# Kernel optimization log

Measured on AMD Instinct MI355X. Metric: run time of the kernel, lower is better.

The kernel has to match this reference:

```python
import jax, jax.numpy as jnp
import numpy as np

E = 1024
H = 16
D = E // H  # projection_dim = 64


def setup_inputs() -> dict:
    key = jax.random.key(0)
    ks = jax.random.split(key, 9)
    s = 1.0 / np.sqrt(E)
    return {
        "inputs": jax.random.normal(ks[0], (2, 2048, E), dtype=jnp.float32),
        "Wq": jax.random.uniform(ks[1], (E, E), jnp.float32, -s, s),
        "bq": jax.random.uniform(ks[2], (E,), jnp.float32, -s, s),
        "Wk": jax.random.uniform(ks[3], (E, E), jnp.float32, -s, s),
        "bk": jax.random.uniform(ks[4], (E,), jnp.float32, -s, s),
        "Wv": jax.random.uniform(ks[5], (E, E), jnp.float32, -s, s),
        "bv": jax.random.uniform(ks[6], (E,), jnp.float32, -s, s),
        "Wo": jax.random.uniform(ks[7], (E, E), jnp.float32, -s, s),
        "bo": jax.random.uniform(ks[8], (E,), jnp.float32, -s, s),
    }


def reference(inputs, Wq, bq, Wk, bk, Wv, bv, Wo, bo):
    B, S, _ = inputs.shape
    # Linear layers use y = x @ W.T + b (torch convention); weights here stored as [E,E]
    q = inputs @ Wq.T + bq
    k = inputs @ Wk.T + bk
    v = inputs @ Wv.T + bv
    # separate heads: [B,S,E] -> [B,H,S,D]
    q = q.reshape(B, S, H, D).transpose(0, 2, 1, 3)
    k = k.reshape(B, S, H, D).transpose(0, 2, 1, 3)
    v = v.reshape(B, S, H, D).transpose(0, 2, 1, 3)
    scale = 1.0 / jnp.sqrt(jnp.float32(D))
    scores = jnp.einsum('bhqd,bhkd->bhqk', q, k) * scale  # [B,H,S,S]
    weights = jax.nn.softmax(scores, axis=-1)
    attn = jnp.einsum('bhqk,bhkd->bhqd', weights, v)  # [B,H,S,D]
    concat = attn.transpose(0, 2, 1, 3).reshape(B, S, E)
    # dropout is identity in eval mode
    return concat @ Wo.T + bo
```

## Files before the change

kernel.cpp:

```cpp
#include <hip/hip_runtime.h>
#include <hip/hip_bf16.h>
#include <stdint.h>

#define E_ 1024
#define H_ 16
#define D_ 64
#define B_ 2
#define S_ 2048
#define M_ 4096

typedef __bf16 bf16_t;
typedef __bf16 bf16x8 __attribute__((ext_vector_type(8)));
typedef __bf16 bf16x4 __attribute__((ext_vector_type(4)));
typedef __bf16 bf16x2 __attribute__((ext_vector_type(2)));
typedef float  f32x4  __attribute__((ext_vector_type(4)));
typedef float  f32x16 __attribute__((ext_vector_type(16)));
typedef unsigned int u32x2 __attribute__((ext_vector_type(2)));
typedef unsigned int u32x4 __attribute__((ext_vector_type(4)));

__global__ __launch_bounds__(256) void cvt_all(
    const float* __restrict__ x,
    const float* __restrict__ w0, const float* __restrict__ w1,
    const float* __restrict__ w2, const float* __restrict__ w3,
    bf16_t* __restrict__ xd,
    bf16_t* __restrict__ d0, bf16_t* __restrict__ d1,
    bf16_t* __restrict__ d2, bf16_t* __restrict__ d3) {
  int i = blockIdx.x * blockDim.x + threadIdx.x;
  const float* src;
  bf16_t* dst;
  int off;
  if (i < (1 << 20)) {
    src = x; dst = xd; off = i;
  } else {
    int j = i - (1 << 20);
    int z = j >> 18;
    off = j & ((1 << 18) - 1);
    src = (z == 0) ? w0 : (z == 1) ? w1 : (z == 2) ? w2 : w3;
    dst = (z == 0) ? d0 : (z == 1) ? d1 : (z == 2) ? d2 : d3;
  }
  float4 v = reinterpret_cast<const float4*>(src)[off];
  bf16x4 o;
  o[0] = (bf16_t)v.x; o[1] = (bf16_t)v.y; o[2] = (bf16_t)v.z; o[3] = (bf16_t)v.w;
  reinterpret_cast<bf16x4*>(dst)[off] = o;
}

static __device__ __forceinline__ void gl_lds16(const bf16_t* g, bf16_t* l) {
  __builtin_amdgcn_global_load_lds((__attribute__((address_space(1))) void*)g,
                                   (__attribute__((address_space(3))) void*)l,
                                   16, 0, 0);
}

template <int SWAP>
static __device__ __forceinline__ void gemm128_mainloop(
    const bf16_t* __restrict__ Ag, const bf16_t* __restrict__ Bg,
    bf16_t* ldsA0, bf16_t* ldsA1, bf16_t* ldsB0, bf16_t* ldsB1,
    int m0, int n0, f32x4 acc[4][4]) {
  const int tid  = threadIdx.x;
  const int lane = tid & 63, wave = tid >> 6;
  const int lrow = lane & 15, lgrp = lane >> 4;
  const int wr = (wave >> 1) * 64, wc = (wave & 1) * 64;
  const int skol = (lane & 3) * 8;
  const int c0 = wave * 2;
  const int rowA = c0 * 16 + (lane >> 2);
  const f32x4 zero = {0.f, 0.f, 0.f, 0.f};
#pragma unroll
  for (int i = 0; i < 4; i++)
#pragma unroll
    for (int j = 0; j < 4; j++) acc[i][j] = zero;

  gl_lds16(Ag + (size_t)(m0 + rowA) * E_ + skol,      ldsA0 + c0 * 512);
  gl_lds16(Ag + (size_t)(m0 + rowA + 16) * E_ + skol, ldsA0 + (c0 + 1) * 512);
  gl_lds16(Bg + (size_t)(n0 + rowA) * E_ + skol,      ldsB0 + c0 * 512);
  gl_lds16(Bg + (size_t)(n0 + rowA + 16) * E_ + skol, ldsB0 + (c0 + 1) * 512);
  __syncthreads();

  for (int kt = 0; kt < E_ / 32; ++kt) {
    bf16_t* sA = (kt & 1) ? ldsA1 : ldsA0;
    bf16_t* sB = (kt & 1) ? ldsB1 : ldsB0;
    if (kt + 1 < E_ / 32) {
      bf16_t* dA = (kt & 1) ? ldsA0 : ldsA1;
      bf16_t* dB = (kt & 1) ? ldsB0 : ldsB1;
      const int k0 = (kt + 1) * 32;
      gl_lds16(Ag + (size_t)(m0 + rowA) * E_ + k0 + skol,      dA + c0 * 512);
      gl_lds16(Ag + (size_t)(m0 + rowA + 16) * E_ + k0 + skol, dA + (c0 + 1) * 512);
      gl_lds16(Bg + (size_t)(n0 + rowA) * E_ + k0 + skol,      dB + c0 * 512);
      gl_lds16(Bg + (size_t)(n0 + rowA + 16) * E_ + k0 + skol, dB + (c0 + 1) * 512);
    }
    bf16x8 fA[4], fB[4];
#pragma unroll
    for (int i = 0; i < 4; i++)
      fA[i] = *reinterpret_cast<const bf16x8*>(sA + (wr + i * 16 + lrow) * 32 + lgrp * 8);
#pragma unroll
    for (int j = 0; j < 4; j++)
      fB[j] = *reinterpret_cast<const bf16x8*>(sB + (wc + j * 16 + lrow) * 32 + lgrp * 8);
#pragma unroll
    for (int i = 0; i < 4; i++)
#pragma unroll
      for (int j = 0; j < 4; j++)
        acc[i][j] = SWAP
          ? __builtin_amdgcn_mfma_f32_16x16x32_bf16(fB[j], fA[i], acc[i][j], 0, 0, 0)
          : __builtin_amdgcn_mfma_f32_16x16x32_bf16(fA[i], fB[j], acc[i][j], 0, 0, 0);
    __syncthreads();
  }
}

__global__ __launch_bounds__(256) void qkv_gemm(
    const bf16_t* __restrict__ xbf, const bf16_t* __restrict__ Wqkv,
    const float* __restrict__ bq, const float* __restrict__ bk, const float* __restrict__ bv,
    bf16_t* __restrict__ Qo, bf16_t* __restrict__ Kf, bf16_t* __restrict__ Vf) {
  __shared__ alignas(16) bf16_t ldsA[2][128 * 32];
  __shared__ alignas(16) bf16_t ldsB[2][128 * 32];
  const int m0 = blockIdx.x * 128, n0 = blockIdx.y * 128;
  const int z = n0 >> 10;
  const float* bias = (z == 0) ? bq : ((z == 1) ? bk : bv);
  const int lane = threadIdx.x & 63, wave = threadIdx.x >> 6;
  const int lrow = lane & 15, lgrp = lane >> 4;
  const int wr = (wave >> 1) * 64, wc = (wave & 1) * 64;
  f32x4 acc[4][4];

  if (z == 2) {
    gemm128_mainloop<0>(xbf, Wqkv, ldsA[0], ldsA[1], ldsB[0], ldsB[1], m0, n0, acc);
#pragma unroll
    for (int i = 0; i < 4; i++) {
      const int mbase = m0 + wr + i * 16 + lgrp * 4;
      const int b = mbase >> 11, kv = mbase & (S_ - 1);
      const int t = kv >> 6, st = (kv >> 4) & 3, hi2 = (kv >> 3) & 1, j0 = kv & 7;
#pragma unroll
      for (int j = 0; j < 4; j++) {
        const int n = (n0 & 1023) + wc + j * 16 + lrow;
        const float bn = bias[n];
        const int h = n >> 6, d = n & 63;
        const int hh = d >> 5, lane2 = (hi2 << 5) | (d & 31);
        bf16x4 v;
#pragma unroll
        for (int r = 0; r < 4; r++) v[r] = (bf16_t)(acc[i][j][r] + bn);
        const size_t off = ((((size_t)(b * H_ + h) * 32 + t) * 8 + hh * 4 + st) * 64 + lane2) * 8 + j0;
        *reinterpret_cast<bf16x4*>(Vf + off) = v;
      }
    }
  } else if (z == 1) {
    gemm128_mainloop<1>(xbf, Wqkv, ldsA[0], ldsA[1], ldsB[0], ldsB[1], m0, n0, acc);
#pragma unroll
    for (int i = 0; i < 4; i++) {
      const int m = m0 + wr + i * 16 + lrow;
      const int b = m >> 11, kv = m & (S_ - 1);
      const int t = kv >> 6, hh = (kv >> 5) & 1, qll = kv & 31;
#pragma unroll
      for (int j = 0; j < 4; j++) {
        const int nb = (n0 & 1023) + wc + j * 16 + lgrp * 4;
        const int h = nb >> 6, d = nb & 63;
        const int ds = d >> 4, hi2 = (d >> 3) & 1, el = d & 7;
        const int lane2 = (hi2 << 5) | qll;
        const f32x4 b4 = *reinterpret_cast<const f32x4*>(bias + nb);
        bf16x4 v;
#pragma unroll
        for (int r = 0; r < 4; r++) v[r] = (bf16_t)(acc[i][j][r] + b4[r]);
        const size_t off = ((((size_t)(b * H_ + h) * 32 + t) * 8 + hh * 4 + ds) * 64 + lane2) * 8 + el;
        *reinterpret_cast<bf16x4*>(Kf + off) = v;
      }
    }
  } else {
    gemm128_mainloop<1>(xbf, Wqkv, ldsA[0], ldsA[1], ldsB[0], ldsB[1], m0, n0, acc);
    const float scale = 0.18033688011112042f;
#pragma unroll
    for (int i = 0; i < 4; i++) {
      const int m = m0 + wr + i * 16 + lrow;
      const int b = m >> 11, s = m & (S_ - 1);
#pragma unroll
      for (int j = 0; j < 4; j++) {
        const int nb = (n0 & 1023) + wc + j * 16 + lgrp * 4;
        const int h = nb >> 6, d = nb & 63;
        const f32x4 b4 = *reinterpret_cast<const f32x4*>(bias + nb);
        bf16x4 v;
#pragma unroll
        for (int r = 0; r < 4; r++) v[r] = (bf16_t)((acc[i][j][r] + b4[r]) * scale);
        *reinterpret_cast<bf16x4*>(Qo + ((size_t)((b * H_ + h) * S_) + s) * D_ + d) = v;
      }
    }
  }
}

__global__ __launch_bounds__(256) void out_gemm(
    const bf16_t* __restrict__ Cbf, const bf16_t* __restrict__ Wob,
    const float* __restrict__ bo, float* __restrict__ out) {
  __shared__ alignas(16) bf16_t ldsA[2][128 * 32];
  __shared__ alignas(16) bf16_t ldsB[2][128 * 32];
  const int m0 = blockIdx.x * 128, n0 = blockIdx.y * 128;
  f32x4 acc[4][4];
  gemm128_mainloop<1>(Cbf, Wob, ldsA[0], ldsA[1], ldsB[0], ldsB[1], m0, n0, acc);

  const int lane = threadIdx.x & 63, wave = threadIdx.x >> 6;
  const int lrow = lane & 15, lgrp = lane >> 4;
  const int wr = (wave >> 1) * 64, wc = (wave & 1) * 64;
#pragma unroll
  for (int i = 0; i < 4; i++) {
    const int m = m0 + wr + i * 16 + lrow;
#pragma unroll
    for (int j = 0; j < 4; j++) {
      const int nb = n0 + wc + j * 16 + lgrp * 4;
      const f32x4 b4 = *reinterpret_cast<const f32x4*>(bo + nb);
      f32x4 v = acc[i][j] + b4;
      *reinterpret_cast<f32x4*>(out + (size_t)m * E_ + nb) = v;
    }
  }
}


static __device__ __forceinline__ unsigned pack2(float a, float b) {
  bf16x2 t; t[0] = (bf16_t)a; t[1] = (bf16_t)b;
  return __builtin_bit_cast(unsigned, t);
}

static __device__ __forceinline__ bf16x8 mkfrag(unsigned a0, unsigned a1,
                                                unsigned a2, unsigned a3) {
  u32x2 s02 = __builtin_amdgcn_permlane32_swap(a0, a2, false, false);
  u32x2 s13 = __builtin_amdgcn_permlane32_swap(a1, a3, false, false);
  u32x4 t; t[0] = s02[0]; t[1] = s13[0]; t[2] = s02[1]; t[3] = s13[1];
  return *reinterpret_cast<bf16x8*>(&t);
}

__global__ __launch_bounds__(512) void attn_kernel(
    const bf16_t* __restrict__ Qg, const bf16_t* __restrict__ Kfg,
    const bf16_t* __restrict__ Vfg, bf16_t* __restrict__ Og) {
  __shared__ alignas(16) f32x4 smO[8 * 256];
  __shared__ float smL[256];
  const int f = blockIdx.x;
  const int bh = (f & 7) * 4 + (f >> 7);
  const int q0 = ((f >> 3) & 15) * 128;
  const int tid = threadIdx.x, lane = tid & 63, wave = tid >> 6;
  const int qsub = wave & 3, kvg = wave >> 2;
  const int ql = lane & 31, hi = lane >> 5;
  const bf16_t* Qb = Qg + (size_t)bh * S_ * D_;
  const bf16x8* Kb = reinterpret_cast<const bf16x8*>(Kfg) + (size_t)bh * 32 * 512 + lane;
  const bf16x8* Vb = reinterpret_cast<const bf16x8*>(Vfg) + (size_t)bh * 32 * 512 + lane;

  const int q = q0 + qsub * 32 + ql;
  bf16x8 qf[4];
#pragma unroll
  for (int ds = 0; ds < 4; ds++)
    qf[ds] = *reinterpret_cast<const bf16x8*>(Qb + (size_t)q * D_ + ds * 16 + hi * 8);

  f32x16 o0, o1;
#pragma unroll
  for (int r = 0; r < 16; r++) { o0[r] = 0.f; o1[r] = 0.f; }
  float li = 0.f;

  for (int it = 0; it < S_ / 128; ++it) {
    const int t = kvg + it * 2;
    const bf16x8* kt = Kb + (size_t)t * 512;
    const bf16x8* vt = Vb + (size_t)t * 512;

    bf16x8 kf0[4], kf1[4];
#pragma unroll
    for (int ds = 0; ds < 4; ds++) { kf0[ds] = kt[ds * 64]; kf1[ds] = kt[(4 + ds) * 64]; }

    f32x16 pa0, pa1;
#pragma unroll
    for (int r = 0; r < 16; r++) { pa0[r] = 0.f; pa1[r] = 0.f; }
    __builtin_amdgcn_s_setprio(1);
#pragma unroll
    for (int ds = 0; ds < 4; ds++) {
      pa0 = __builtin_amdgcn_mfma_f32_32x32x16_bf16(kf0[ds], qf[ds], pa0, 0, 0, 0);
      pa1 = __builtin_amdgcn_mfma_f32_32x32x16_bf16(kf1[ds], qf[ds], pa1, 0, 0, 0);
    }
    __builtin_amdgcn_s_setprio(0);

    bf16x8 vf0[4], vf1[4];
#pragma unroll
    for (int st = 0; st < 4; st++) { vf0[st] = vt[st * 64]; vf1[st] = vt[(4 + st) * 64]; }

    float ps = 0.f;
#pragma unroll
    for (int r = 0; r < 16; r++) {
      pa0[r] = __builtin_amdgcn_exp2f(pa0[r]); ps += pa0[r];
      pa1[r] = __builtin_amdgcn_exp2f(pa1[r]); ps += pa1[r];
    }
    {
      u32x2 ss = __builtin_amdgcn_permlane32_swap(
          __builtin_bit_cast(unsigned, ps), __builtin_bit_cast(unsigned, ps), false, false);
      ps = __builtin_bit_cast(float, ss[0]) + __builtin_bit_cast(float, ss[1]);
    }
    li += ps;

    unsigned w0[8], w1[8];
#pragma unroll
    for (int i = 0; i < 8; i++) {
      w0[i] = pack2(pa0[2 * i], pa0[2 * i + 1]);
      w1[i] = pack2(pa1[2 * i], pa1[2 * i + 1]);
    }
    bf16x8 bfr[4];
    bfr[0] = mkfrag(w0[0], w0[1], w0[2], w0[3]);
    bfr[1] = mkfrag(w0[4], w0[5], w0[6], w0[7]);
    bfr[2] = mkfrag(w1[0], w1[1], w1[2], w1[3]);
    bfr[3] = mkfrag(w1[4], w1[5], w1[6], w1[7]);

    __builtin_amdgcn_s_setprio(1);
#pragma unroll
    for (int st = 0; st < 4; st++) {
      o0 = __builtin_amdgcn_mfma_f32_32x32x16_bf16(vf0[st], bfr[st], o0, 0, 0, 0);
      o1 = __builtin_amdgcn_mfma_f32_32x32x16_bf16(vf1[st], bfr[st], o1, 0, 0, 0);
    }
    __builtin_amdgcn_s_setprio(0);
  }

  const int mi_ = qsub * 64 + lane;
  if (kvg == 1) {
#pragma unroll
    for (int g = 0; g < 4; g++) {
      f32x4 a;
#pragma unroll
      for (int i = 0; i < 4; i++) a[i] = o0[g * 4 + i];
      smO[g * 256 + mi_] = a;
    }
#pragma unroll
    for (int g = 0; g < 4; g++) {
      f32x4 a;
#pragma unroll
      for (int i = 0; i < 4; i++) a[i] = o1[g * 4 + i];
      smO[(g + 4) * 256 + mi_] = a;
    }
    smL[mi_] = li;
  }
  __syncthreads();
  if (kvg == 0) {
    li += smL[mi_];
#pragma unroll
    for (int g = 0; g < 4; g++) {
      f32x4 a = smO[g * 256 + mi_];
#pragma unroll
      for (int i = 0; i < 4; i++) o0[g * 4 + i] += a[i];
    }
#pragma unroll
    for (int g = 0; g < 4; g++) {
      f32x4 a = smO[(g + 4) * 256 + mi_];
#pragma unroll
      for (int i = 0; i < 4; i++) o1[g * 4 + i] += a[i];
    }
    const float inv = 1.0f / li;
    const int b = bh >> 4, h = bh & 15;
    bf16_t* orow = Og + (size_t)(b * S_ + q) * E_ + h * 64;
#pragma unroll
    for (int g = 0; g < 4; g++) {
      bf16x4 v;
#pragma unroll
      for (int i = 0; i < 4; i++) v[i] = (bf16_t)(o0[g * 4 + i] * inv);
      *reinterpret_cast<bf16x4*>(orow + g * 8 + hi * 4) = v;
    }
#pragma unroll
    for (int g = 0; g < 4; g++) {
      bf16x4 v;
#pragma unroll
      for (int i = 0; i < 4; i++) v[i] = (bf16_t)(o1[g * 4 + i] * inv);
      *reinterpret_cast<bf16x4*>(orow + 32 + g * 8 + hi * 4) = v;
    }
  }
}

extern "C" void kernel_launch(void* const* d_in, const int* in_sizes, int n_in,
                              void* d_out, int out_size, void* d_ws, size_t ws_size,
                              hipStream_t stream) {
  (void)in_sizes; (void)n_in; (void)out_size; (void)ws_size;
  const float* x  = (const float*)d_in[0];
  const float* Wq = (const float*)d_in[1];
  const float* bq = (const float*)d_in[2];
  const float* Wk = (const float*)d_in[3];
  const float* bk = (const float*)d_in[4];
  const float* Wv = (const float*)d_in[5];
  const float* bv = (const float*)d_in[6];
  const float* Wo = (const float*)d_in[7];
  const float* bo = (const float*)d_in[8];
  float* out = (float*)d_out;

  bf16_t* ws  = (bf16_t*)d_ws;
  bf16_t* xbf = ws;
  bf16_t* Ct  = ws;
  bf16_t* wqb = ws + (4u << 20);
  bf16_t* wkb = ws + (5u << 20);
  bf16_t* wvb = ws + (6u << 20);
  bf16_t* wob = ws + (7u << 20);
  bf16_t* Qt  = ws + (8u << 20);
  bf16_t* Kf  = ws + (12u << 20);
  bf16_t* Vf  = ws + (16u << 20);

  cvt_all<<<8192, 256, 0, stream>>>(x, Wq, Wk, Wv, Wo, xbf, wqb, wkb, wvb, wob);

  qkv_gemm<<<dim3(32, 24), 256, 0, stream>>>(xbf, wqb, bq, bk, bv, Qt, Kf, Vf);
  attn_kernel<<<512, 512, 0, stream>>>(Qt, Kf, Vf, Ct);
  out_gemm<<<dim3(32, 8), 256, 0, stream>>>(Ct, wob, bo, out);
}
```

Baseline: 115.3 us.

## Split attention KV range four ways with 64-query blocks and tree reduction

Each attention block now covers 64 queries instead of 128 and splits the key/value sequence across four wave groups instead of two. The launch grid doubles to 1024 blocks. Partial outputs and row sums are combined by a two-stage reduction through shared memory. This is meant to give more blocks to fill the GPU's compute units and more parallelism per query, at the cost of more Q reloads, more K/V traffic per query and an extra barrier with LDS reduction.

```diff
diff --git a/kernel.cpp b/kernel.cpp
--- a/kernel.cpp
+++ b/kernel.cpp
@@ -222,13 +222,14 @@
 __global__ __launch_bounds__(512) void attn_kernel(
     const bf16_t* __restrict__ Qg, const bf16_t* __restrict__ Kfg,
     const bf16_t* __restrict__ Vfg, bf16_t* __restrict__ Og) {
-  __shared__ alignas(16) f32x4 smO[8 * 256];
-  __shared__ float smL[256];
+  __shared__ alignas(16) f32x4 smO[2][8][128];
+  __shared__ float smL[2][128];
   const int f = blockIdx.x;
-  const int bh = (f & 7) * 4 + (f >> 7);
-  const int q0 = ((f >> 3) & 15) * 128;
+  const int inner = f >> 3;
+  const int bh = (f & 7) * 4 + (inner >> 5);
+  const int q0 = (inner & 31) * 64;
   const int tid = threadIdx.x, lane = tid & 63, wave = tid >> 6;
-  const int qsub = wave & 3, kvg = wave >> 2;
+  const int qsub = wave & 1, kvg = wave >> 1;
   const int ql = lane & 31, hi = lane >> 5;
   const bf16_t* Qb = Qg + (size_t)bh * S_ * D_;
   const bf16x8* Kb = reinterpret_cast<const bf16x8*>(Kfg) + (size_t)bh * 32 * 512 + lane;
@@ -245,8 +246,8 @@
   for (int r = 0; r < 16; r++) { o0[r] = 0.f; o1[r] = 0.f; }
   float li = 0.f;
 
-  for (int it = 0; it < S_ / 128; ++it) {
-    const int t = kvg + it * 2;
+  for (int it = 0; it < S_ / 256; ++it) {
+    const int t = kvg + it * 4;
     const bf16x8* kt = Kb + (size_t)t * 512;
     const bf16x8* vt = Vb + (size_t)t * 512;
 
@@ -303,36 +304,70 @@
     __builtin_amdgcn_s_setprio(0);
   }
 
-  const int mi_ = qsub * 64 + lane;
+  const int idx = qsub * 64 + lane;
+  if (kvg >= 2) {
+    const int slot = kvg - 2;
+#pragma unroll
+    for (int g = 0; g < 4; g++) {
+      f32x4 a;
+#pragma unroll
+      for (int i = 0; i < 4; i++) a[i] = o0[g * 4 + i];
+      smO[slot][g][idx] = a;
+    }
+#pragma unroll
+    for (int g = 0; g < 4; g++) {
+      f32x4 a;
+#pragma unroll
+      for (int i = 0; i < 4; i++) a[i] = o1[g * 4 + i];
+      smO[slot][g + 4][idx] = a;
+    }
+    smL[slot][idx] = li;
+  }
+  __syncthreads();
+  if (kvg < 2) {
+    li += smL[kvg][idx];
+#pragma unroll
+    for (int g = 0; g < 4; g++) {
+      f32x4 a = smO[kvg][g][idx];
+#pragma unroll
+      for (int i = 0; i < 4; i++) o0[g * 4 + i] += a[i];
+    }
+#pragma unroll
+    for (int g = 0; g < 4; g++) {
+      f32x4 a = smO[kvg][g + 4][idx];
+#pragma unroll
+      for (int i = 0; i < 4; i++) o1[g * 4 + i] += a[i];
+    }
+  }
   if (kvg == 1) {
 #pragma unroll
     for (int g = 0; g < 4; g++) {
       f32x4 a;
 #pragma unroll
       for (int i = 0; i < 4; i++) a[i] = o0[g * 4 + i];
-      smO[g * 256 + mi_] = a;
+      smO[1][g][idx] = a;
     }
 #pragma unroll
     for (int g = 0; g < 4; g++) {
       f32x4 a;
 #pragma unroll
       for (int i = 0; i < 4; i++) a[i] = o1[g * 4 + i];
-      smO[(g + 4) * 256 + mi_] = a;
-    }
-    smL[mi_] = li;
+      smO[1][g + 4][idx] = a;
+    }
+    smL[1][idx] = li;
   }
   __syncthreads();
   if (kvg == 0) {
-    li += smL[mi_];
-#pragma unroll
-    for (int g = 0; g < 4; g++) {
-      f32x4 a = smO[g * 256 + mi_];
+    li += smL[1][idx];
+#pragma unroll
+    for (int g = 0; g < 4; g++) {
+      f32x4 a = smO[1][g][idx];
 #pragma unroll
       for (int i = 0; i < 4; i++) o0[g * 4 + i] += a[i];
     }
 #pragma unroll
     for (int g = 0; g < 4; g++) {
-      f32x4 a = smO[(g + 4) * 256 + mi_];
+      f32x4 a = smO[1][g + 4][idx];
 #pragma unroll
       for (int i = 0; i < 4; i++) o1[g * 4 + i] += a[i];
     }
@@ -385,6 +420,6 @@
   cvt_all<<<8192, 256, 0, stream>>>(x, Wq, Wk, Wv, Wo, xbf, wqb, wkb, wvb, wob);
 
   qkv_gemm<<<dim3(32, 24), 256, 0, stream>>>(xbf, wqb, bq, bk, bv, Qt, Kf, Vf);
-  attn_kernel<<<512, 512, 0, stream>>>(Qt, Kf, Vf, Ct);
+  attn_kernel<<<1024, 512, 0, stream>>>(Qt, Kf, Vf, Ct);
   out_gemm<<<dim3(32, 8), 256, 0, stream>>>(Ct, wob, bo, out);
 }
```

Result: slower. 118.8 us (+3.0%).

## Share K/V tiles via double-buffered LDS across 256-query attention blocks

Applied to the files above, without the earlier changes.

The attention kernel now processes 256 queries per block, with all 8 waves working on different query rows instead of splitting the KV range across two wave groups. Each K/V tile is loaded once into double-buffered shared memory with async global-to-LDS copies and reused by all waves, which removes the cross-wave reduction of partial outputs. This cuts redundant global/L2 reads of K and V. In exchange the grid is halved to 256 blocks, which may underfill the GPU, and each tile iteration adds a barrier.

```diff
diff --git a/kernel.cpp b/kernel.cpp
--- a/kernel.cpp
+++ b/kernel.cpp
@@ -222,19 +222,19 @@
 __global__ __launch_bounds__(512) void attn_kernel(
     const bf16_t* __restrict__ Qg, const bf16_t* __restrict__ Kfg,
     const bf16_t* __restrict__ Vfg, bf16_t* __restrict__ Og) {
-  __shared__ alignas(16) f32x4 smO[8 * 256];
-  __shared__ float smL[256];
+  __shared__ alignas(16) bf16_t Kl[2][4096];
+  __shared__ alignas(16) bf16_t Vl[2][4096];
   const int f = blockIdx.x;
-  const int bh = (f & 7) * 4 + (f >> 7);
-  const int q0 = ((f >> 3) & 15) * 128;
+  const int j = f >> 3;
+  const int bh = (f & 7) * 4 + (j >> 3);
+  const int q0 = (j & 7) * 256;
   const int tid = threadIdx.x, lane = tid & 63, wave = tid >> 6;
-  const int qsub = wave & 3, kvg = wave >> 2;
   const int ql = lane & 31, hi = lane >> 5;
   const bf16_t* Qb = Qg + (size_t)bh * S_ * D_;
-  const bf16x8* Kb = reinterpret_cast<const bf16x8*>(Kfg) + (size_t)bh * 32 * 512 + lane;
-  const bf16x8* Vb = reinterpret_cast<const bf16x8*>(Vfg) + (size_t)bh * 32 * 512 + lane;
-
-  const int q = q0 + qsub * 32 + ql;
+  const bf16_t* Kb = Kfg + (size_t)bh * 32 * 4096;
+  const bf16_t* Vb = Vfg + (size_t)bh * 32 * 4096;
+
+  const int q = q0 + wave * 32 + ql;
   bf16x8 qf[4];
 #pragma unroll
   for (int ds = 0; ds < 4; ds++)
@@ -245,14 +245,23 @@
   for (int r = 0; r < 16; r++) { o0[r] = 0.f; o1[r] = 0.f; }
   float li = 0.f;
 
-  for (int it = 0; it < S_ / 128; ++it) {
-    const int t = kvg + it * 2;
-    const bf16x8* kt = Kb + (size_t)t * 512;
-    const bf16x8* vt = Vb + (size_t)t * 512;
+  gl_lds16(Kb + tid * 8, &Kl[0][tid * 8]);
+  gl_lds16(Vb + tid * 8, &Vl[0][tid * 8]);
+  __syncthreads();
+
+  for (int t = 0; t < 32; ++t) {
+    const int cur = t & 1;
+    if (t + 1 < 32) {
+      gl_lds16(Kb + (size_t)(t + 1) * 4096 + tid * 8, &Kl[cur ^ 1][tid * 8]);
+      gl_lds16(Vb + (size_t)(t + 1) * 4096 + tid * 8, &Vl[cur ^ 1][tid * 8]);
+    }
 
     bf16x8 kf0[4], kf1[4];
 #pragma unroll
-    for (int ds = 0; ds < 4; ds++) { kf0[ds] = kt[ds * 64]; kf1[ds] = kt[(4 + ds) * 64]; }
+    for (int ds = 0; ds < 4; ds++) {
+      kf0[ds] = *reinterpret_cast<const bf16x8*>(&Kl[cur][(ds * 64 + lane) * 8]);
+      kf1[ds] = *reinterpret_cast<const bf16x8*>(&Kl[cur][((4 + ds) * 64 + lane) * 8]);
+    }
 
     f32x16 pa0, pa1;
 #pragma unroll
@@ -267,7 +276,10 @@
 
     bf16x8 vf0[4], vf1[4];
 #pragma unroll
-    for (int st = 0; st < 4; st++) { vf0[st] = vt[st * 64]; vf1[st] = vt[(4 + st) * 64]; }
+    for (int st = 0; st < 4; st++) {
+      vf0[st] = *reinterpret_cast<const bf16x8*>(&Vl[cur][(st * 64 + lane) * 8]);
+      vf1[st] = *reinterpret_cast<const bf16x8*>(&Vl[cur][((4 + st) * 64 + lane) * 8]);
+    }
 
     float ps = 0.f;
 #pragma unroll
@@ -301,58 +313,26 @@
       o1 = __builtin_amdgcn_mfma_f32_32x32x16_bf16(vf1[st], bfr[st], o1, 0, 0, 0);
     }
     __builtin_amdgcn_s_setprio(0);
-  }
-
-  const int mi_ = qsub * 64 + lane;
-  if (kvg == 1) {
-#pragma unroll
-    for (int g = 0; g < 4; g++) {
-      f32x4 a;
-#pragma unroll
-      for (int i = 0; i < 4; i++) a[i] = o0[g * 4 + i];
-      smO[g * 256 + mi_] = a;
-    }
-#pragma unroll
-    for (int g = 0; g < 4; g++) {
-      f32x4 a;
-#pragma unroll
-      for (int i = 0; i < 4; i++) a[i] = o1[g * 4 + i];
-      smO[(g + 4) * 256 + mi_] = a;
-    }
-    smL[mi_] = li;
-  }
-  __syncthreads();
-  if (kvg == 0) {
-    li += smL[mi_];
-#pragma unroll
-    for (int g = 0; g < 4; g++) {
-      f32x4 a = smO[g * 256 + mi_];
-#pragma unroll
-      for (int i = 0; i < 4; i++) o0[g * 4 + i] += a[i];
-    }
-#pragma unroll
-    for (int g = 0; g < 4; g++) {
-      f32x4 a = smO[(g + 4) * 256 + mi_];
-#pragma unroll
-      for (int i = 0; i < 4; i++) o1[g * 4 + i] += a[i];
-    }
-    const float inv = 1.0f / li;
-    const int b = bh >> 4, h = bh & 15;
-    bf16_t* orow = Og + (size_t)(b * S_ + q) * E_ + h * 64;
-#pragma unroll
-    for (int g = 0; g < 4; g++) {
-      bf16x4 v;
-#pragma unroll
-      for (int i = 0; i < 4; i++) v[i] = (bf16_t)(o0[g * 4 + i] * inv);
-      *reinterpret_cast<bf16x4*>(orow + g * 8 + hi * 4) = v;
-    }
-#pragma unroll
-    for (int g = 0; g < 4; g++) {
-      bf16x4 v;
-#pragma unroll
-      for (int i = 0; i < 4; i++) v[i] = (bf16_t)(o1[g * 4 + i] * inv);
-      *reinterpret_cast<bf16x4*>(orow + 32 + g * 8 + hi * 4) = v;
-    }
+
+    __syncthreads();
+  }
+
+  const float inv = 1.0f / li;
+  const int b = bh >> 4, h = bh & 15;
+  bf16_t* orow = Og + (size_t)(b * S_ + q) * E_ + h * 64;
+#pragma unroll
+  for (int g = 0; g < 4; g++) {
+    bf16x4 v;
+#pragma unroll
+    for (int i = 0; i < 4; i++) v[i] = (bf16_t)(o0[g * 4 + i] * inv);
+    *reinterpret_cast<bf16x4*>(orow + g * 8 + hi * 4) = v;
+  }
+#pragma unroll
+  for (int g = 0; g < 4; g++) {
+    bf16x4 v;
+#pragma unroll
+    for (int i = 0; i < 4; i++) v[i] = (bf16_t)(o1[g * 4 + i] * inv);
+    *reinterpret_cast<bf16x4*>(orow + 32 + g * 8 + hi * 4) = v;
   }
 }
 
@@ -385,6 +365,6 @@
   cvt_all<<<8192, 256, 0, stream>>>(x, Wq, Wk, Wv, Wo, xbf, wqb, wkb, wvb, wob);
 
   qkv_gemm<<<dim3(32, 24), 256, 0, stream>>>(xbf, wqb, bq, bk, bv, Qt, Kf, Vf);
-  attn_kernel<<<512, 512, 0, stream>>>(Qt, Kf, Vf, Ct);
+  attn_kernel<<<256, 512, 0, stream>>>(Qt, Kf, Vf, Ct);
   out_gemm<<<dim3(32, 8), 256, 0, stream>>>(Ct, wob, bo, out);
 }
```

After: 116.5 us. Within noise of the previous version (+1.0%).
